# Optimization experiments

Hardware: AMD Instinct MI355X
Metric: run time of the kernel (lower is better)

## Reference

```python
import jax, jax.numpy as jnp
import numpy as np
import math

DIM = 1024
N_HEADS = 16
HEAD_DIM = DIM // N_HEADS
MAX_SEQ_LEN = 2048


def rope_tables(seq_len, head_dim):
    inv_freq = 1.0 / (10000.0 ** (jnp.arange(0, head_dim, 2, dtype=jnp.float32) / head_dim))
    t = jnp.arange(seq_len, dtype=jnp.float32)
    freqs = jnp.einsum('i,j->ij', t, inv_freq)          # [T, D/2]
    emb = jnp.concatenate([freqs, freqs], axis=-1)      # [T, D]
    return jnp.cos(emb), jnp.sin(emb)


def rotate_half(x):
    x1, x2 = jnp.split(x, 2, axis=-1)
    return jnp.concatenate([-x2, x1], axis=-1)


def setup_inputs() -> dict:
    key = jax.random.key(0)
    k1, k2, k3 = jax.random.split(key, 3)
    B, T = 4, 2048
    x = jax.random.normal(k1, (B, T, DIM), dtype=jnp.float32)
    # Linear(dim, 3*dim, bias=False) and Linear(dim, dim, bias=False); stored as [in, out]
    Wqkv = jax.random.normal(k2, (DIM, 3 * DIM), dtype=jnp.float32) * (1.0 / math.sqrt(DIM))
    Wproj = jax.random.normal(k3, (DIM, DIM), dtype=jnp.float32) * (1.0 / math.sqrt(DIM))
    return {"x": x, "Wqkv": Wqkv, "Wproj": Wproj}


def reference(x, Wqkv, Wproj):
    B, T, C = x.shape
    qkv = x @ Wqkv                                       # [B,T,3C]
    q, k, v = jnp.split(qkv, 3, axis=-1)
    # [B,T,C] -> [B,H,T,D]
    def to_heads(t_):
        return t_.reshape(B, T, N_HEADS, HEAD_DIM).transpose(0, 2, 1, 3)
    q, k, v = to_heads(q), to_heads(k), to_heads(v)
    cos, sin = rope_tables(T, HEAD_DIM)                  # [T,D]
    cos = cos[None, None, :, :]
    sin = sin[None, None, :, :]
    q = q * cos + rotate_half(q) * sin
    k = k * cos + rotate_half(k) * sin
    scale = 1.0 / math.sqrt(HEAD_DIM)
    att = jnp.einsum('bhqd,bhkd->bhqk', q, k) * scale    # [B,H,T,T]
    causal = jnp.triu(jnp.ones((T, T), dtype=bool), k=1)
    att = jnp.where(causal[None, None], -jnp.inf, att)
    att = jax.nn.softmax(att, axis=-1)
    y = jnp.einsum('bhqk,bhkd->bhqd', att, v)            # [B,H,T,D]
    y = y.transpose(0, 2, 1, 3).reshape(B, T, C)
    return y @ Wproj
```

## Files before the change

### kernel.cpp

```cpp
#include <hip/hip_runtime.h>
#include <hip/hip_bf16.h>

typedef unsigned short u16;
typedef __attribute__((ext_vector_type(8))) short short8;
typedef __attribute__((ext_vector_type(4))) float floatx4;

__device__ __forceinline__ u16 f2bf(float f) {
    union { float f; unsigned u; } v; v.f = f;
    unsigned r = v.u + 0x7fffu + ((v.u >> 16) & 1u);
    return (u16)(r >> 16);
}
__device__ __forceinline__ float fexp2(float x) {
#if __has_builtin(__builtin_amdgcn_exp2f)
    return __builtin_amdgcn_exp2f(x);
#else
    return exp2f(x);
#endif
}
__device__ __forceinline__ unsigned cvtpk_bf16(float lo, float hi) {
    unsigned r;
    asm("v_cvt_pk_bf16_f32 %0, %1, %2" : "=v"(r) : "v"(lo), "v"(hi));
    return r;
}
__device__ __forceinline__ void permlane32_swap(unsigned &a, unsigned &b) {
    asm("v_permlane32_swap_b32 %0, %1" : "+v"(a), "+v"(b));
}
__device__ __forceinline__ void permlane16_swap(unsigned &a, unsigned &b) {
    asm("v_permlane16_swap_b32 %0, %1" : "+v"(a), "+v"(b));
}

__device__ __forceinline__ void async_load16(const void* g, void* l) {
    __builtin_amdgcn_global_load_lds(
        (const __attribute__((address_space(1))) unsigned int*)g,
        (__attribute__((address_space(3))) unsigned int*)l, 16, 0, 0);
}

#define B_   4
#define T_   2048
#define NH_  16
#define HD_  64
#define DIM_ 1024
#define M_   (B_ * T_)
#define NQKV (3 * DIM_)
#define NT_  16
#define LOG2E 1.4426950408889634f

__global__ void cvt_x(const float* __restrict__ in, u16* __restrict__ out) {
    int idx = blockIdx.x * 256 + threadIdx.x;
    float4 v = ((const float4*)in)[idx];
    ushort4 o;
    o.x = f2bf(v.x); o.y = f2bf(v.y); o.z = f2bf(v.z); o.w = f2bf(v.w);
    ((ushort4*)out)[idx] = o;
}

__global__ void transpose_cvt(const float* __restrict__ in, u16* __restrict__ out,
                              int R, int Cn) {
    __shared__ float tile[32][33];
    int c0 = blockIdx.x * 32, r0 = blockIdx.y * 32;
    int tx = threadIdx.x, ty = threadIdx.y;
#pragma unroll
    for (int i = 0; i < 4; ++i)
        tile[ty + i * 8][tx] = in[(size_t)(r0 + ty + i * 8) * Cn + c0 + tx];
    __syncthreads();
#pragma unroll
    for (int i = 0; i < 4; ++i)
        out[(size_t)(c0 + ty + i * 8) * R + r0 + tx] = f2bf(tile[tx][ty + i * 8]);
}

__global__ void rope_table(float* __restrict__ tabc, float* __restrict__ tabs) {
    int idx = blockIdx.x * 256 + threadIdx.x;
    if (idx >= T_ * 32) return;
    int t = idx >> 5, j = idx & 31;
    double invf = pow(10000.0, -(double)j / 32.0);
    double th = (double)t * invf;
    tabc[idx] = (float)cos(th);
    tabs[idx] = (float)sin(th);
}

__global__ void v_transpose(const u16* __restrict__ Vh, u16* __restrict__ Vt) {
    __shared__ u16 tile[64 * 68];
    const int tid = threadIdx.x;
    const int bh = blockIdx.y, b = bh >> 4, h = bh & 15;
    const int t0 = blockIdx.x * 64;
    {
        int lr = tid >> 2;
        int lc = tid & 3;
        const u16* src = Vh + ((size_t)(b * T_ + t0 + lr)) * DIM_ + h * HD_;
#pragma unroll
        for (int j = 0; j < 4; ++j) {
            int c = (lc + j * 4) * 4;
            *(uint2*)&tile[lr * 68 + c] = *(const uint2*)(src + c);
        }
    }
    __syncthreads();
    {
        int d2 = tid >> 3, tseg = tid & 7;
        u16 lo8[8], hi8[8];
#pragma unroll
        for (int j = 0; j < 8; ++j) {
            unsigned w = *(const unsigned*)&tile[(tseg * 8 + j) * 68 + d2 * 2];
            lo8[j] = (u16)(w & 0xffffu);
            hi8[j] = (u16)(w >> 16);
        }
        size_t ob = ((size_t)bh * HD_ + 2 * d2) * T_ + t0 + tseg * 8;
        *(uint4*)(Vt + ob) = *(const uint4*)lo8;
        *(uint4*)(Vt + ob + T_) = *(const uint4*)hi8;
    }
}

__device__ __forceinline__ void gemm_core(const u16* __restrict__ A,
                                          const u16* __restrict__ Bt,
                                          u16* smem, int m0, int n0, int tid,
                                          floatx4 (&acc)[4][4]) {
    const int wave = tid >> 6, lane = tid & 63;
    const int ln15 = lane & 15, quad = lane >> 4;
    const int wm = (wave & 1) * 64, wn = (wave >> 1) * 64;
    const int l8 = lane & 7, ld8 = lane >> 3;
    const int sgc = (l8 ^ ld8) * 8;
    const int K = DIM_;

    const u16* aS = A + (size_t)(m0 + wave * 16 + ld8) * K + sgc;
    const u16* bS = Bt + (size_t)(n0 + wave * 32 + ld8) * K + sgc;

    auto issueA_B0 = [&](int k2, u16* As2, u16* Bs2) {
        async_load16(aS + k2,          As2 + (wave * 16) * 64);
        async_load16(aS + 8 * K + k2,  As2 + (wave * 16 + 8) * 64);
        async_load16(bS + k2,          Bs2 + (wave * 32) * 64);
    };
    auto issueB123 = [&](int k2, u16* Bs2) {
        async_load16(bS + 8 * K + k2,  Bs2 + (wave * 32 + 8) * 64);
        async_load16(bS + 16 * K + k2, Bs2 + (wave * 32 + 16) * 64);
        async_load16(bS + 24 * K + k2, Bs2 + (wave * 32 + 24) * 64);
    };
    auto compute = [&](const u16* As_c, const u16* Bs_c, int c4) {
        short8 af[4], bfv[4];
#pragma unroll
        for (int i = 0; i < 4; ++i) {
            int row = wm + i * 16 + ln15;
            af[i] = *(const short8*)&As_c[row * 64 + (((c4 + quad) ^ (row & 7)) << 3)];
        }
#pragma unroll
        for (int j = 0; j < 4; ++j) {
            int row = wn + j * 16 + ln15;
            bfv[j] = *(const short8*)&Bs_c[row * 64 + (((c4 + quad) ^ (row & 7)) << 3)];
        }
        __builtin_amdgcn_s_setprio(1);
#pragma unroll
        for (int i = 0; i < 4; ++i)
#pragma unroll
            for (int j = 0; j < 4; ++j)
                acc[i][j] = __builtin_amdgcn_mfma_f32_16x16x32_bf16(
                    af[i], bfv[j], acc[i][j], 0, 0, 0);
        __builtin_amdgcn_s_setprio(0);
    };

    issueA_B0(0, smem, smem + 24576);
    issueB123(0, smem + 24576);
    issueA_B0(64, smem + 8192, smem + 24576 + 16384);
    issueB123(64, smem + 24576 + 16384);

#pragma unroll 1
    for (int t = 0; t < NT_; ++t) {
        if (t < NT_ - 1) asm volatile("s_waitcnt vmcnt(6)" ::: "memory");
        else             asm volatile("s_waitcnt vmcnt(0)" ::: "memory");
        __builtin_amdgcn_s_barrier();
        asm volatile("" ::: "memory");

        const int cb = t % 3, cb2 = (t + 2) % 3;
        const u16* As_c = smem + cb * 8192;
        const u16* Bs_c = smem + 24576 + cb * 16384;
        u16* As2 = smem + cb2 * 8192;
        u16* Bs2 = smem + 24576 + cb2 * 16384;
        const bool iss = t < NT_ - 2;
        const int k2 = (t + 2) * 64;

        if (iss) issueA_B0(k2, As2, Bs2);
        compute(As_c, Bs_c, 0);
        asm volatile("" ::: "memory");
        __builtin_amdgcn_s_barrier();
        asm volatile("" ::: "memory");

        if (iss) issueB123(k2, Bs2);
        compute(As_c, Bs_c, 4);
        asm volatile("" ::: "memory");
    }
}

__global__ __launch_bounds__(512, 2) void gemm_qkv(const u16* __restrict__ A,
                                                   const u16* __restrict__ Bt,
                                                   const float* __restrict__ tabc,
                                                   const float* __restrict__ tabs,
                                                   u16* __restrict__ Qo,
                                                   u16* __restrict__ Ko,
                                                   u16* __restrict__ Vh) {
    __shared__ __align__(16) u16 smem[73728];
    const int tid = threadIdx.x;
    const int bid = blockIdx.x;
    const int wg = (bid & 7) * 96 + (bid >> 3);
    const int bx = wg / 64, by = wg - bx * 64;
    const int m0 = by * 128, n0 = bx * 256;

    floatx4 acc[4][4] = {};
    gemm_core(A, Bt, smem, m0, n0, tid, acc);

    const int wave = tid >> 6, lane = tid & 63;
    const int ln15 = lane & 15, quad = lane >> 4;
    const int wm = (wave & 1) * 64, wn = (wave >> 1) * 64;

    __syncthreads();
    u16* Es = smem;
    const int sel = n0 >> 10;
    auto es_put = [&](int row, int col, u16 v) {
        int c = col >> 3;
        int pc = (c & 24) | ((c & 7) ^ (row & 7));
        Es[row * 256 + pc * 8 + (col & 7)] = v;
    };
    if (sel == 2) {
#pragma unroll
        for (int i = 0; i < 4; ++i)
#pragma unroll
            for (int j = 0; j < 4; ++j)
#pragma unroll
                for (int r = 0; r < 4; ++r)
                    es_put(wm + i * 16 + quad * 4 + r, wn + j * 16 + ln15,
                           f2bf(acc[i][j][r]));
    } else {
        const float scale = sel ? 1.0f : 0.125f * LOG2E;
#pragma unroll
        for (int i = 0; i < 4; ++i)
#pragma unroll
            for (int jjl = 0; jjl < 2; ++jjl) {
                int j = jjl * 16 + ln15;
#pragma unroll
                for (int r = 0; r < 4; ++r) {
                    int row = wm + i * 16 + quad * 4 + r;
                    int t = (m0 + row) & (T_ - 1);
                    float cs = tabc[t * 32 + j], sn = tabs[t * 32 + j];
                    float xl = acc[i][jjl][r], xh = acc[i][jjl + 2][r];
                    es_put(row, wn + j,      f2bf((xl * cs - xh * sn) * scale));
                    es_put(row, wn + j + 32, f2bf((xh * cs + xl * sn) * scale));
                }
            }
    }
    __syncthreads();
    const int bb = m0 >> 11;
    u16* outqk = (sel == 1) ? Ko : Qo;
#pragma unroll
    for (int k = 0; k < 8; ++k) {
        int cid = tid + k * 512;
        int row = cid >> 5, c = cid & 31;
        int pc = (c & 24) | ((c & 7) ^ (row & 7));
        uint4 v = *(const uint4*)&Es[row * 256 + pc * 8];
        if (sel == 2) {
            *(uint4*)&Vh[(size_t)(m0 + row) * DIM_ + (n0 & 1023) + c * 8] = v;
        } else {
            int h = ((n0 & 1023) >> 6) + (c >> 3);
            int d = (c & 7) * 8;
            int t = (m0 + row) & (T_ - 1);
            *(uint4*)&outqk[((size_t)(bb * NH_ + h) * T_ + t) * HD_ + d] = v;
        }
    }
}

__global__ __launch_bounds__(512, 2) void gemm_proj(const u16* __restrict__ A,
                                                    const u16* __restrict__ Bt,
                                                    float* __restrict__ C) {
    __shared__ __align__(16) u16 smem[73728];
    const int tid = threadIdx.x;
    const int bid = blockIdx.x;
    const int wg = (bid & 7) * 32 + (bid >> 3);
    const int bx = wg / 64, by = wg - bx * 64;
    const int m0 = by * 128, n0 = bx * 256;

    floatx4 acc[4][4] = {};
    gemm_core(A, Bt, smem, m0, n0, tid, acc);

    const int wave = tid >> 6, lane = tid & 63;
    const int ln15 = lane & 15, quad = lane >> 4;
    const int wm = (wave & 1) * 64, wn = (wave >> 1) * 64;
#pragma unroll
    for (int i = 0; i < 4; ++i)
#pragma unroll
        for (int j = 0; j < 4; ++j)
#pragma unroll
            for (int r = 0; r < 4; ++r) {
                int m = m0 + wm + i * 16 + quad * 4 + r;
                int n = n0 + wn + j * 16 + ln15;
                C[(size_t)m * DIM_ + n] = acc[i][j][r];
            }
}

__global__ __launch_bounds__(256, 5) void attn_kernel(const u16* __restrict__ Q,
                                                      const u16* __restrict__ Kh,
                                                      const u16* __restrict__ Vt,
                                                      u16* __restrict__ Y) {
    __shared__ __align__(16) u16 Kl[2][64 * 64];
    __shared__ __align__(16) u16 Vl[2][64 * 64];
    const int tid = threadIdx.x, wave = tid >> 6, lane = tid & 63;
    const int ln15 = lane & 15, quad = lane >> 4;
    const int bid = blockIdx.x;
    const int wg = (bid & 7) * 128 + (bid >> 3);
    const int p = wg & 15;
    const int bh = wg >> 4;
    const int b = bh >> 4, h = bh & 15;
    const int l8 = lane & 7, ld8 = lane >> 3;
    const int sgc = l8 ^ ld8;

    const u16* kbase = Kh + (size_t)bh * T_ * HD_;
    const u16* vbase = Vt + (size_t)bh * HD_ * T_;
    const short8 ones = {0x3F80, 0x3F80, 0x3F80, 0x3F80,
                         0x3F80, 0x3F80, 0x3F80, 0x3F80};
    const int srow = wave * 16;

#pragma unroll
    for (int half = 0; half < 2; ++half) {
        const int tidx = half ? p : (31 - p);
        const int q0 = tidx * 64;
        const int bm = q0 + srow;

        const u16* qp = Q + ((size_t)bh * T_ + bm + ln15) * HD_;
        short8 qf0 = *(const short8*)(qp + quad * 8);
        short8 qf1 = *(const short8*)(qp + 32 + quad * 8);

        floatx4 o[5] = {};

        __syncthreads();
#pragma unroll
        for (int it = 0; it < 2; ++it) {
            int r = srow + it * 8;
            async_load16(kbase + (size_t)(r + ld8) * HD_ + sgc * 8, &Kl[0][r * 64]);
            async_load16(vbase + (size_t)(r + ld8) * T_ + sgc * 8, &Vl[0][r * 64]);
        }

        for (int kt = 0; kt <= tidx; ++kt) {
            const int cur = kt & 1;
            __syncthreads();
            if (kt < tidx) {
                const int kn = (kt + 1) * 64;
#pragma unroll
                for (int it = 0; it < 2; ++it) {
                    int r = srow + it * 8;
                    async_load16(kbase + (size_t)(kn + r + ld8) * HD_ + sgc * 8,
                                 &Kl[cur ^ 1][r * 64]);
                    async_load16(vbase + (size_t)(r + ld8) * T_ + kn + sgc * 8,
                                 &Vl[cur ^ 1][r * 64]);
                }
            }
            floatx4 s[4] = {};
            __builtin_amdgcn_s_setprio(1);
#pragma unroll
            for (int nt = 0; nt < 4; ++nt) {
                int row = nt * 16 + ln15;
                short8 kf0 = *(const short8*)&Kl[cur][row * 64 + ((quad ^ (row & 7)) << 3)];
                short8 kf1 = *(const short8*)&Kl[cur][row * 64 + (((4 + quad) ^ (row & 7)) << 3)];
                s[nt] = __builtin_amdgcn_mfma_f32_16x16x32_bf16(kf0, qf0, s[nt], 0, 0, 0);
                s[nt] = __builtin_amdgcn_mfma_f32_16x16x32_bf16(kf1, qf1, s[nt], 0, 0, 0);
            }
            __builtin_amdgcn_s_setprio(0);
            if (kt == tidx) {
                const int lim = srow + ln15;
#pragma unroll
                for (int nt = 0; nt < 4; ++nt) {
                    int key = nt * 16 + quad * 4;
#pragma unroll
                    for (int r = 0; r < 4; ++r)
                        s[nt][r] = (key + r > lim) ? 0.f : fexp2(s[nt][r]);
                }
            } else {
#pragma unroll
                for (int nt = 0; nt < 4; ++nt)
#pragma unroll
                    for (int r = 0; r < 4; ++r) s[nt][r] = fexp2(s[nt][r]);
            }
            unsigned x0 = cvtpk_bf16(s[0][0], s[0][1]);
            unsigned x1 = cvtpk_bf16(s[1][0], s[1][1]);
            unsigned y0 = cvtpk_bf16(s[0][2], s[0][3]);
            unsigned y1 = cvtpk_bf16(s[1][2], s[1][3]);
            unsigned x2 = cvtpk_bf16(s[2][0], s[2][1]);
            unsigned x3 = cvtpk_bf16(s[3][0], s[3][1]);
            unsigned y2 = cvtpk_bf16(s[2][2], s[2][3]);
            unsigned y3 = cvtpk_bf16(s[3][2], s[3][3]);
            permlane32_swap(x0, x1); permlane16_swap(x0, x1);
            permlane32_swap(y0, y1); permlane16_swap(y0, y1);
            permlane32_swap(x2, x3); permlane16_swap(x2, x3);
            permlane32_swap(y2, y3); permlane16_swap(y2, y3);
            union { unsigned u[4]; short8 s8; } pk0, pk1;
            pk0.u[0] = x0; pk0.u[1] = y0; pk0.u[2] = x1; pk0.u[3] = y1;
            pk1.u[0] = x2; pk1.u[1] = y2; pk1.u[2] = x3; pk1.u[3] = y3;
            __builtin_amdgcn_s_setprio(1);
#pragma unroll
            for (int nt = 0; nt < 4; ++nt) {
                int row = nt * 16 + ln15;
                short8 vf0 = *(const short8*)&Vl[cur][row * 64 + ((quad ^ (row & 7)) << 3)];
                short8 vf1 = *(const short8*)&Vl[cur][row * 64 + (((4 + quad) ^ (row & 7)) << 3)];
                o[nt] = __builtin_amdgcn_mfma_f32_16x16x32_bf16(pk0.s8, vf0, o[nt], 0, 0, 0);
                o[nt] = __builtin_amdgcn_mfma_f32_16x16x32_bf16(pk1.s8, vf1, o[nt], 0, 0, 0);
            }
            o[4] = __builtin_amdgcn_mfma_f32_16x16x32_bf16(pk0.s8, ones, o[4], 0, 0, 0);
            o[4] = __builtin_amdgcn_mfma_f32_16x16x32_bf16(pk1.s8, ones, o[4], 0, 0, 0);
            __builtin_amdgcn_s_setprio(0);
        }
#pragma unroll
        for (int r = 0; r < 4; ++r) {
            float inv = 1.f / o[4][r];
            int row = bm + quad * 4 + r;
            u16* yp = Y + ((size_t)(b * T_ + row)) * DIM_ + h * HD_;
#pragma unroll
            for (int nt = 0; nt < 4; ++nt)
                yp[nt * 16 + ln15] = f2bf(o[nt][r] * inv);
        }
    }
}

extern "C" void kernel_launch(void* const* d_in, const int* in_sizes, int n_in,
                              void* d_out, int out_size, void* d_ws, size_t ws_size,
                              hipStream_t stream) {
    const float* x     = (const float*)d_in[0];
    const float* Wqkv  = (const float*)d_in[1];
    const float* Wproj = (const float*)d_in[2];
    float* out = (float*)d_out;
    char* ws = (char*)d_ws;

    const size_t SZ_XB  = (size_t)M_ * DIM_ * 2;
    const size_t SZ_WQT = (size_t)NQKV * DIM_ * 2;
    const size_t SZ_WPT = (size_t)DIM_ * DIM_ * 2;
    const size_t SZ_Q   = SZ_XB;
    const size_t SZ_TAB = (size_t)T_ * 32 * 4;

    u16*   xb   = (u16*)(ws);
    u16*   wqt  = (u16*)(ws + SZ_XB);
    u16*   wpt  = (u16*)(ws + SZ_XB + SZ_WQT);
    u16*   qb   = (u16*)(ws + SZ_XB + SZ_WQT + SZ_WPT);
    u16*   kb   = (u16*)(ws + SZ_XB + SZ_WQT + SZ_WPT + SZ_Q);
    u16*   vhb  = (u16*)(ws + SZ_XB + SZ_WQT + SZ_WPT + 2 * SZ_Q);
    u16*   vtb  = (u16*)(ws + SZ_XB + SZ_WQT + SZ_WPT + 3 * SZ_Q);
    float* tabc = (float*)(ws + SZ_XB + SZ_WQT + SZ_WPT + 4 * SZ_Q);
    float* tabs = (float*)(ws + SZ_XB + SZ_WQT + SZ_WPT + 4 * SZ_Q + SZ_TAB);
    u16*   yb   = xb;

    rope_table<<<(T_ * 32 + 255) / 256, 256, 0, stream>>>(tabc, tabs);
    cvt_x<<<(M_ * DIM_ / 4) / 256, 256, 0, stream>>>(x, xb);
    transpose_cvt<<<dim3(NQKV / 32, DIM_ / 32), dim3(32, 8), 0, stream>>>(Wqkv, wqt, DIM_, NQKV);
    transpose_cvt<<<dim3(DIM_ / 32, DIM_ / 32), dim3(32, 8), 0, stream>>>(Wproj, wpt, DIM_, DIM_);
    gemm_qkv<<<768, 512, 0, stream>>>(xb, wqt, tabc, tabs, qb, kb, vhb);
    v_transpose<<<dim3(T_ / 64, B_ * NH_), 256, 0, stream>>>(vhb, vtb);
    attn_kernel<<<1024, 256, 0, stream>>>(qb, kb, vtb, yb);
    gemm_proj<<<256, 512, 0, stream>>>(yb, wpt, out);
}
```

Baseline: 239.9 us.

## Shrink GEMM tiles to 128x128 with 4 waves and double buffering

Replaces the 128x256 tile, 8-wave, triple-buffered GEMM core with a 128x128 tile, 4-wave, double-buffered core. LDS per block drops from 144KB to 64KB and launch bounds become (256,4), giving more blocks per CU and twice as many blocks overall. The block-to-tile mapping also changes to group M tiles for L2 reuse. In exchange, each tile reuses operands less, and the simpler pipeline waits for all loads (vmcnt(0)) every iteration, which can expose memory latency.

Measured after the change: 240.9 us. No clear change (+0.4%).

```diff
diff --git a/kernel.cpp b/kernel.cpp
--- a/kernel.cpp
+++ b/kernel.cpp
@@ -108,10 +108,10 @@
     }
 }
 
-__device__ __forceinline__ void gemm_core(const u16* __restrict__ A,
-                                          const u16* __restrict__ Bt,
-                                          u16* smem, int m0, int n0, int tid,
-                                          floatx4 (&acc)[4][4]) {
+__device__ __forceinline__ void gemm_core128(const u16* __restrict__ A,
+                                             const u16* __restrict__ Bt,
+                                             u16* smem, int m0, int n0, int tid,
+                                             floatx4 (&acc)[4][4]) {
     const int wave = tid >> 6, lane = tid & 63;
     const int ln15 = lane & 15, quad = lane >> 4;
     const int wm = (wave & 1) * 64, wn = (wave >> 1) * 64;
@@ -119,30 +119,29 @@
     const int sgc = (l8 ^ ld8) * 8;
     const int K = DIM_;
 
-    const u16* aS = A + (size_t)(m0 + wave * 16 + ld8) * K + sgc;
+    const u16* aS = A + (size_t)(m0 + wave * 32 + ld8) * K + sgc;
     const u16* bS = Bt + (size_t)(n0 + wave * 32 + ld8) * K + sgc;
 
-    auto issueA_B0 = [&](int k2, u16* As2, u16* Bs2) {
-        async_load16(aS + k2,          As2 + (wave * 16) * 64);
-        async_load16(aS + 8 * K + k2,  As2 + (wave * 16 + 8) * 64);
-        async_load16(bS + k2,          Bs2 + (wave * 32) * 64);
+    auto stage = [&](int k0, u16* buf) {
+#pragma unroll
+        for (int it = 0; it < 4; ++it) {
+            async_load16(aS + (size_t)(it * 8) * K + k0,
+                         buf + (wave * 32 + it * 8) * 64);
+            async_load16(bS + (size_t)(it * 8) * K + k0,
+                         buf + 8192 + (wave * 32 + it * 8) * 64);
+        }
     };
-    auto issueB123 = [&](int k2, u16* Bs2) {
-        async_load16(bS + 8 * K + k2,  Bs2 + (wave * 32 + 8) * 64);
-        async_load16(bS + 16 * K + k2, Bs2 + (wave * 32 + 16) * 64);
-        async_load16(bS + 24 * K + k2, Bs2 + (wave * 32 + 24) * 64);
-    };
-    auto compute = [&](const u16* As_c, const u16* Bs_c, int c4) {
+    auto compute = [&](const u16* buf, int c4) {
         short8 af[4], bfv[4];
 #pragma unroll
         for (int i = 0; i < 4; ++i) {
             int row = wm + i * 16 + ln15;
-            af[i] = *(const short8*)&As_c[row * 64 + (((c4 + quad) ^ (row & 7)) << 3)];
+            af[i] = *(const short8*)&buf[row * 64 + (((c4 + quad) ^ (row & 7)) << 3)];
         }
 #pragma unroll
         for (int j = 0; j < 4; ++j) {
             int row = wn + j * 16 + ln15;
-            bfv[j] = *(const short8*)&Bs_c[row * 64 + (((c4 + quad) ^ (row & 7)) << 3)];
+            bfv[j] = *(const short8*)&buf[8192 + row * 64 + (((c4 + quad) ^ (row & 7)) << 3)];
         }
         __builtin_amdgcn_s_setprio(1);
 #pragma unroll
@@ -154,54 +153,37 @@
         __builtin_amdgcn_s_setprio(0);
     };
 
-    issueA_B0(0, smem, smem + 24576);
-    issueB123(0, smem + 24576);
-    issueA_B0(64, smem + 8192, smem + 24576 + 16384);
-    issueB123(64, smem + 24576 + 16384);
-
+    stage(0, smem);
 #pragma unroll 1
     for (int t = 0; t < NT_; ++t) {
-        if (t < NT_ - 1) asm volatile("s_waitcnt vmcnt(6)" ::: "memory");
-        else             asm volatile("s_waitcnt vmcnt(0)" ::: "memory");
+        asm volatile("s_waitcnt vmcnt(0)" ::: "memory");
         __builtin_amdgcn_s_barrier();
         asm volatile("" ::: "memory");
-
-        const int cb = t % 3, cb2 = (t + 2) % 3;
-        const u16* As_c = smem + cb * 8192;
-        const u16* Bs_c = smem + 24576 + cb * 16384;
-        u16* As2 = smem + cb2 * 8192;
-        u16* Bs2 = smem + 24576 + cb2 * 16384;
-        const bool iss = t < NT_ - 2;
-        const int k2 = (t + 2) * 64;
-
-        if (iss) issueA_B0(k2, As2, Bs2);
-        compute(As_c, Bs_c, 0);
+        if (t + 1 < NT_) stage((t + 1) * 64, smem + ((t + 1) & 1) * 16384);
+        const u16* cur = smem + (t & 1) * 16384;
+        compute(cur, 0);
+        compute(cur, 4);
         asm volatile("" ::: "memory");
-        __builtin_amdgcn_s_barrier();
-        asm volatile("" ::: "memory");
-
-        if (iss) issueB123(k2, Bs2);
-        compute(As_c, Bs_c, 4);
-        asm volatile("" ::: "memory");
-    }
-}
-
-__global__ __launch_bounds__(512, 2) void gemm_qkv(const u16* __restrict__ A,
+    }
+}
+
+__global__ __launch_bounds__(256, 4) void gemm_qkv(const u16* __restrict__ A,
                                                    const u16* __restrict__ Bt,
                                                    const float* __restrict__ tabc,
                                                    const float* __restrict__ tabs,
                                                    u16* __restrict__ Qo,
                                                    u16* __restrict__ Ko,
                                                    u16* __restrict__ Vh) {
-    __shared__ __align__(16) u16 smem[73728];
+    __shared__ __align__(16) u16 smem[32768];
     const int tid = threadIdx.x;
     const int bid = blockIdx.x;
-    const int wg = (bid & 7) * 96 + (bid >> 3);
-    const int bx = wg / 64, by = wg - bx * 64;
-    const int m0 = by * 128, n0 = bx * 256;
+    const int local = bid >> 3;
+    const int by = (bid & 7) * 8 + (local & 7);
+    const int bx = local >> 3;
+    const int m0 = by * 128, n0 = bx * 128;
 
     floatx4 acc[4][4] = {};
-    gemm_core(A, Bt, smem, m0, n0, tid, acc);
+    gemm_core128(A, Bt, smem, m0, n0, tid, acc);
 
     const int wave = tid >> 6, lane = tid & 63;
     const int ln15 = lane & 15, quad = lane >> 4;
@@ -212,18 +194,18 @@
     const int sel = n0 >> 10;
     auto es_put = [&](int row, int col, u16 v) {
         int c = col >> 3;
-        int pc = (c & 24) | ((c & 7) ^ (row & 7));
-        Es[row * 256 + pc * 8 + (col & 7)] = v;
+        int pc = (c & 8) | ((c & 7) ^ (row & 7));
+        Es[row * 128 + pc * 8 + (col & 7)] = v;
     };
     if (sel == 2) {
 #pragma unroll
         for (int i = 0; i < 4; ++i)
 #pragma unroll
-            for (int j = 0; j < 4; ++j)
+            for (int jj = 0; jj < 4; ++jj)
 #pragma unroll
                 for (int r = 0; r < 4; ++r)
-                    es_put(wm + i * 16 + quad * 4 + r, wn + j * 16 + ln15,
-                           f2bf(acc[i][j][r]));
+                    es_put(wm + i * 16 + quad * 4 + r, wn + jj * 16 + ln15,
+                           f2bf(acc[i][jj][r]));
     } else {
         const float scale = sel ? 1.0f : 0.125f * LOG2E;
 #pragma unroll
@@ -247,10 +229,10 @@
     u16* outqk = (sel == 1) ? Ko : Qo;
 #pragma unroll
     for (int k = 0; k < 8; ++k) {
-        int cid = tid + k * 512;
-        int row = cid >> 5, c = cid & 31;
-        int pc = (c & 24) | ((c & 7) ^ (row & 7));
-        uint4 v = *(const uint4*)&Es[row * 256 + pc * 8];
+        int cid = tid + k * 256;
+        int row = cid >> 4, c = cid & 15;
+        int pc = (c & 8) | ((c & 7) ^ (row & 7));
+        uint4 v = *(const uint4*)&Es[row * 128 + pc * 8];
         if (sel == 2) {
             *(uint4*)&Vh[(size_t)(m0 + row) * DIM_ + (n0 & 1023) + c * 8] = v;
         } else {
@@ -262,18 +244,19 @@
     }
 }
 
-__global__ __launch_bounds__(512, 2) void gemm_proj(const u16* __restrict__ A,
+__global__ __launch_bounds__(256, 4) void gemm_proj(const u16* __restrict__ A,
                                                     const u16* __restrict__ Bt,
                                                     float* __restrict__ C) {
-    __shared__ __align__(16) u16 smem[73728];
+    __shared__ __align__(16) u16 smem[32768];
     const int tid = threadIdx.x;
     const int bid = blockIdx.x;
-    const int wg = (bid & 7) * 32 + (bid >> 3);
-    const int bx = wg / 64, by = wg - bx * 64;
-    const int m0 = by * 128, n0 = bx * 256;
+    const int local = bid >> 3;
+    const int by = (bid & 7) * 8 + (local & 7);
+    const int bx = local >> 3;
+    const int m0 = by * 128, n0 = bx * 128;
 
     floatx4 acc[4][4] = {};
-    gemm_core(A, Bt, smem, m0, n0, tid, acc);
+    gemm_core128(A, Bt, smem, m0, n0, tid, acc);
 
     const int wave = tid >> 6, lane = tid & 63;
     const int ln15 = lane & 15, quad = lane >> 4;
@@ -281,12 +264,12 @@
 #pragma unroll
     for (int i = 0; i < 4; ++i)
 #pragma unroll
-        for (int j = 0; j < 4; ++j)
+        for (int jj = 0; jj < 4; ++jj)
 #pragma unroll
             for (int r = 0; r < 4; ++r) {
                 int m = m0 + wm + i * 16 + quad * 4 + r;
-                int n = n0 + wn + j * 16 + ln15;
-                C[(size_t)m * DIM_ + n] = acc[i][j][r];
+                int n = n0 + wn + jj * 16 + ln15;
+                C[(size_t)m * DIM_ + n] = acc[i][jj][r];
             }
 }
 
@@ -442,8 +425,8 @@
     cvt_x<<<(M_ * DIM_ / 4) / 256, 256, 0, stream>>>(x, xb);
     transpose_cvt<<<dim3(NQKV / 32, DIM_ / 32), dim3(32, 8), 0, stream>>>(Wqkv, wqt, DIM_, NQKV);
     transpose_cvt<<<dim3(DIM_ / 32, DIM_ / 32), dim3(32, 8), 0, stream>>>(Wproj, wpt, DIM_, DIM_);
-    gemm_qkv<<<768, 512, 0, stream>>>(xb, wqt, tabc, tabs, qb, kb, vhb);
+    gemm_qkv<<<1536, 256, 0, stream>>>(xb, wqt, tabc, tabs, qb, kb, vhb);
     v_transpose<<<dim3(T_ / 64, B_ * NH_), 256, 0, stream>>>(vhb, vtb);
     attn_kernel<<<1024, 256, 0, stream>>>(qb, kb, vtb, yb);
-    gemm_proj<<<256, 512, 0, stream>>>(yb, wpt, out);
-}
+    gemm_proj<<<512, 256, 0, stream>>>(yb, wpt, out);
+}
```
